# Performance work log

Hardware: AMD Instinct MI355X
Metric: run time of the kernel (lower is better)

Reference implementation:

```python
import jax, jax.numpy as jnp
import numpy as np

BN_EPS = 1e-5
LRELU_SLOPE = 0.2  # CBL = Conv1d(k=1) + BatchNorm1d + LeakyReLU


def three_nn(xyz1, xyz2):
    # xyz1: (B,N,3), xyz2: (B,M,3) -> squared dists (B,N,3), idx (B,N,3)
    d2 = (jnp.sum(xyz1 ** 2, -1, keepdims=True)
          + jnp.sum(xyz2 ** 2, -1)[:, None, :]
          - 2.0 * jnp.einsum('bnd,bmd->bnm', xyz1, xyz2))  # (B,N,M)
    neg, idx = jax.lax.top_k(-d2, 3)
    return -neg, idx


def three_interpolate(points2, idx, weight):
    # points2: (B,C,M), idx: (B,N,3), weight: (B,N,3) -> (B,C,N)
    gathered = jax.vmap(lambda p, i: p[:, i])(points2, idx)  # (B,C,N,3)
    return jnp.einsum('bcnk,bnk->bcn', gathered, weight)


def cbl(x, W, b, gamma, beta):
    # x: (B,C,N); 1x1 conv -> BN (training-mode stats) -> LeakyReLU
    y = jnp.einsum('oc,bcn->bon', W, x) + b[None, :, None]
    mean = jnp.mean(y, axis=(0, 2), keepdims=True)
    var = jnp.var(y, axis=(0, 2), keepdims=True)
    y = (y - mean) * jax.lax.rsqrt(var + BN_EPS)
    y = gamma[None, :, None] * y + beta[None, :, None]
    return jnp.where(y >= 0, y, LRELU_SLOPE * y)


def setup_inputs() -> dict:
    key = jax.random.key(0)
    ks = jax.random.split(key, 8)
    B, N, M = 4, 8192, 2048
    C1, C2 = 128, 256
    Cin = C2 + C1  # use_points1=True -> concat
    H = 256
    return {
        'xyz1': jax.random.normal(ks[0], (B, N, 3), jnp.float32),
        'xyz2': jax.random.normal(ks[1], (B, M, 3), jnp.float32),
        'points1': jax.random.normal(ks[2], (B, C1, N), jnp.float32),
        'points2': jax.random.normal(ks[3], (B, C2, M), jnp.float32),
        'W1': jax.random.normal(ks[4], (H, Cin), jnp.float32) * (1.0 / np.sqrt(Cin)),
        'b1': jnp.zeros((H,), jnp.float32),
        'gamma1': jnp.ones((H,), jnp.float32),
        'beta1': jnp.zeros((H,), jnp.float32),
        'W2': jax.random.normal(ks[5], (H, H), jnp.float32) * (1.0 / np.sqrt(H)),
        'b2': jnp.zeros((H,), jnp.float32),
        'gamma2': jnp.ones((H,), jnp.float32),
        'beta2': jnp.zeros((H,), jnp.float32),
    }


def reference(xyz1, xyz2, points1, points2, W1, b1, gamma1, beta1, W2, b2, gamma2, beta2):
    dist, idx = three_nn(xyz1, xyz2)
    dist = jnp.maximum(dist, 1e-10)
    recip = 1.0 / dist
    weight = recip / jnp.sum(recip, axis=2, keepdims=True)  # (B,N,3)
    interp = three_interpolate(points2, idx, weight)        # (B,C2,N)
    new_points = jnp.concatenate([interp, points1], axis=1)  # (B,C2+C1,N)
    new_points = cbl(new_points, W1, b1, gamma1, beta1)
    new_points = cbl(new_points, W2, b2, gamma2, beta2)
    return new_points
```

## Files before the change

### kernel.cpp

```cpp
#include <hip/hip_runtime.h>
#include <math.h>

constexpr int B   = 4;
constexpr int N   = 8192;
constexpr int M   = 2048;
constexpr int C1  = 128;
constexpr int C2  = 256;
constexpr int HCH = 256;
constexpr int CIN = 384;
constexpr float BN_EPS = 1e-5f;
constexpr float SLOPE  = 0.2f;
constexpr float BN_CNT = (float)(B * N);

__global__ void k_zero(float* __restrict__ stats) {
  int i = blockIdx.x * blockDim.x + threadIdx.x;
  if (i < 1024) stats[i] = 0.f;
}

__global__ __launch_bounds__(256) void k_nn(const float* __restrict__ xyz1,
                                            const float* __restrict__ xyz2,
                                            float* __restrict__ wgt,
                                            int* __restrict__ idxo) {
  __shared__ float4 q[4][512];
  __shared__ float  md[4][64][3];
  __shared__ int    mi[4][64][3];
  const int tid = threadIdx.x;
  const int b   = blockIdx.y;
  const int n0  = blockIdx.x * 64;

  const float* src = xyz2 + (size_t)b * M * 3;
  for (int i = tid; i < M; i += 256) {
    float x = src[i*3+0], y = src[i*3+1], z = src[i*3+2];
    q[i >> 9][i & 511] = make_float4(x, y, z, x*x + y*y + z*z);
  }
  __syncthreads();

  const int w = tid >> 6;
  const int t = tid & 63;
  const int n = n0 + t;
  const float* p = xyz1 + ((size_t)b * N + n) * 3;
  const float px = p[0], py = p[1], pz = p[2];
  const float n1 = px*px + py*py + pz*pz;

  float d0 = 3.4e38f, d1 = 3.4e38f, d2 = 3.4e38f;
  int   j0 = 0, j1 = 0, j2 = 0;
  const float4* qs = q[w];
  #pragma unroll 4
  for (int r = 0; r < 512; ++r) {
    float4 c = qs[r];
    float dot = px*c.x + py*c.y + pz*c.z;
    float d = fmaf(-2.f, dot, n1 + c.w);
    if (d < d2) {
      int m = (w << 9) + r;
      if (d < d1) {
        if (d < d0) { d2 = d1; j2 = j1; d1 = d0; j1 = j0; d0 = d; j0 = m; }
        else        { d2 = d1; j2 = j1; d1 = d;  j1 = m; }
      } else        { d2 = d;  j2 = m; }
    }
  }
  md[w][t][0] = d0; md[w][t][1] = d1; md[w][t][2] = d2;
  mi[w][t][0] = j0; mi[w][t][1] = j1; mi[w][t][2] = j2;
  __syncthreads();

  if (tid < 64) {
    float e0 = 3.4e38f, e1 = 3.4e38f, e2 = 3.4e38f;
    int   i0 = 0, i1 = 0, i2 = 0;
    #pragma unroll
    for (int s = 0; s < 4; ++s) {
      #pragma unroll
      for (int k = 0; k < 3; ++k) {
        float d = md[s][tid][k];
        int   m = mi[s][tid][k];
        if (d < e2) {
          if (d < e1) {
            if (d < e0) { e2 = e1; i2 = i1; e1 = e0; i1 = i0; e0 = d; i0 = m; }
            else        { e2 = e1; i2 = i1; e1 = d;  i1 = m; }
          } else        { e2 = d;  i2 = m; }
        }
      }
    }
    e0 = fmaxf(e0, 1e-10f); e1 = fmaxf(e1, 1e-10f); e2 = fmaxf(e2, 1e-10f);
    float r0 = 1.f / e0, r1 = 1.f / e1, r2 = 1.f / e2;
    float s  = r0 + r1 + r2;
    size_t base = ((size_t)b * N + n0 + tid) * 3;
    wgt[base+0] = r0 / s;  wgt[base+1] = r1 / s;  wgt[base+2] = r2 / s;
    idxo[base+0] = i0;     idxo[base+1] = i1;     idxo[base+2] = i2;
  }
}

__global__ __launch_bounds__(256) void k_tr(const float* __restrict__ P2,
                                            float* __restrict__ P2T) {
  __shared__ float t[32][33];
  const int b  = blockIdx.z;
  const int m0 = blockIdx.x * 32;
  const int c0 = blockIdx.y * 32;
  const int tx = threadIdx.x & 31;
  const int ty = threadIdx.x >> 5;
  const float* src = P2 + (size_t)b * C2 * M;
  #pragma unroll
  for (int j = 0; j < 4; ++j)
    t[ty + j*8][tx] = src[(size_t)(c0 + ty + j*8) * M + m0 + tx];
  __syncthreads();
  float* dst = P2T + (size_t)b * M * C2;
  #pragma unroll
  for (int j = 0; j < 4; ++j)
    dst[(size_t)(m0 + ty + j*8) * C2 + c0 + tx] = t[tx][ty + j*8];
}

__global__ __launch_bounds__(256) void k_interp(const float* __restrict__ P2T,
                                                const float* __restrict__ points1,
                                                const float* __restrict__ wgt,
                                                const int* __restrict__ idx,
                                                float* __restrict__ X) {
  const int b = blockIdx.y;
  const int n = blockIdx.x * 256 + threadIdx.x;
  const size_t base = (size_t)b * N + n;
  const int i0 = idx[base*3+0], i1 = idx[base*3+1], i2 = idx[base*3+2];
  const float w0 = wgt[base*3+0], w1 = wgt[base*3+1], w2 = wgt[base*3+2];
  const float4* r0 = (const float4*)(P2T + ((size_t)b * M + i0) * C2);
  const float4* r1 = (const float4*)(P2T + ((size_t)b * M + i1) * C2);
  const float4* r2 = (const float4*)(P2T + ((size_t)b * M + i2) * C2);
  float* Xb = X + (size_t)b * CIN * N + n;
  #pragma unroll 4
  for (int c4 = 0; c4 < C2/4; ++c4) {
    float4 a0 = r0[c4], a1 = r1[c4], a2 = r2[c4];
    Xb[(size_t)(c4*4+0) * N] = w0*a0.x + w1*a1.x + w2*a2.x;
    Xb[(size_t)(c4*4+1) * N] = w0*a0.y + w1*a1.y + w2*a2.y;
    Xb[(size_t)(c4*4+2) * N] = w0*a0.z + w1*a1.z + w2*a2.z;
    Xb[(size_t)(c4*4+3) * N] = w0*a0.w + w1*a1.w + w2*a2.w;
  }
  const float* p1 = points1 + (size_t)b * C1 * N + n;
  float* Xc = Xb + (size_t)C2 * N;
  #pragma unroll 4
  for (int c = 0; c < C1; ++c) Xc[(size_t)c * N] = p1[(size_t)c * N];
}

template <int K, bool XFORM>
__global__ __launch_bounds__(256) void k_gemm(const float* __restrict__ Wm,
                                              const float* __restrict__ bias,
                                              const float* __restrict__ Xin,
                                              const float* __restrict__ coef,
                                              float* __restrict__ Yout,
                                              float* __restrict__ stats) {
  constexpr int BK = 32;
  __shared__ float Wt[BK][64];
  __shared__ float Xt[BK][64];
  const int tid = threadIdx.x;
  const int tx = tid & 15, ty = tid >> 4;
  const int n0 = blockIdx.x * 64;
  const int o0 = blockIdx.y * 64;
  const int b  = blockIdx.z;
  const float* Xb = Xin + (size_t)b * K * N;

  float acc[4][4] = {};

  for (int k0 = 0; k0 < K; k0 += BK) {
    {
      const int o  = tid >> 2;
      const int kk = (tid & 3) * 8;
      const float* wp = Wm + (size_t)(o0 + o) * K + k0 + kk;
      float4 wv0 = *(const float4*)(wp);
      float4 wv1 = *(const float4*)(wp + 4);
      Wt[kk+0][o] = wv0.x; Wt[kk+1][o] = wv0.y; Wt[kk+2][o] = wv0.z; Wt[kk+3][o] = wv0.w;
      Wt[kk+4][o] = wv1.x; Wt[kk+5][o] = wv1.y; Wt[kk+6][o] = wv1.z; Wt[kk+7][o] = wv1.w;
    }
    {
      const int k  = tid >> 3;
      const int nn = (tid & 7) * 8;
      const float* xp = Xb + (size_t)(k0 + k) * N + n0 + nn;
      float4 x0 = *(const float4*)(xp);
      float4 x1 = *(const float4*)(xp + 4);
      if constexpr (XFORM) {
        const float a  = coef[k0 + k];
        const float bb = coef[256 + k0 + k];
        float t;
        t = fmaf(a, x0.x, bb); x0.x = t >= 0.f ? t : SLOPE * t;
        t = fmaf(a, x0.y, bb); x0.y = t >= 0.f ? t : SLOPE * t;
        t = fmaf(a, x0.z, bb); x0.z = t >= 0.f ? t : SLOPE * t;
        t = fmaf(a, x0.w, bb); x0.w = t >= 0.f ? t : SLOPE * t;
        t = fmaf(a, x1.x, bb); x1.x = t >= 0.f ? t : SLOPE * t;
        t = fmaf(a, x1.y, bb); x1.y = t >= 0.f ? t : SLOPE * t;
        t = fmaf(a, x1.z, bb); x1.z = t >= 0.f ? t : SLOPE * t;
        t = fmaf(a, x1.w, bb); x1.w = t >= 0.f ? t : SLOPE * t;
      }
      *(float4*)&Xt[k][nn]     = x0;
      *(float4*)&Xt[k][nn + 4] = x1;
    }
    __syncthreads();
    #pragma unroll
    for (int kk = 0; kk < BK; ++kk) {
      float4 av = *(const float4*)&Wt[kk][ty * 4];
      float4 bv = *(const float4*)&Xt[kk][tx * 4];
      acc[0][0] = fmaf(av.x, bv.x, acc[0][0]);
      acc[0][1] = fmaf(av.x, bv.y, acc[0][1]);
      acc[0][2] = fmaf(av.x, bv.z, acc[0][2]);
      acc[0][3] = fmaf(av.x, bv.w, acc[0][3]);
      acc[1][0] = fmaf(av.y, bv.x, acc[1][0]);
      acc[1][1] = fmaf(av.y, bv.y, acc[1][1]);
      acc[1][2] = fmaf(av.y, bv.z, acc[1][2]);
      acc[1][3] = fmaf(av.y, bv.w, acc[1][3]);
      acc[2][0] = fmaf(av.z, bv.x, acc[2][0]);
      acc[2][1] = fmaf(av.z, bv.y, acc[2][1]);
      acc[2][2] = fmaf(av.z, bv.z, acc[2][2]);
      acc[2][3] = fmaf(av.z, bv.w, acc[2][3]);
      acc[3][0] = fmaf(av.w, bv.x, acc[3][0]);
      acc[3][1] = fmaf(av.w, bv.y, acc[3][1]);
      acc[3][2] = fmaf(av.w, bv.z, acc[3][2]);
      acc[3][3] = fmaf(av.w, bv.w, acc[3][3]);
    }
    __syncthreads();
  }

  #pragma unroll
  for (int i = 0; i < 4; ++i) {
    const int o = o0 + ty * 4 + i;
    const float bi = bias[o];
    float4 v = make_float4(acc[i][0] + bi, acc[i][1] + bi, acc[i][2] + bi, acc[i][3] + bi);
    *(float4*)&Yout[((size_t)b * HCH + o) * N + n0 + tx * 4] = v;
    float s = v.x + v.y + v.z + v.w;
    float qq = v.x*v.x + v.y*v.y + v.z*v.z + v.w*v.w;
    #pragma unroll
    for (int off = 1; off < 16; off <<= 1) {
      s  += __shfl_xor(s, off);
      qq += __shfl_xor(qq, off);
    }
    if (tx == 0) {
      atomicAdd(&stats[o], s);
      atomicAdd(&stats[256 + o], qq);
    }
  }
}

__global__ void k_fin(const float* __restrict__ stats,
                      const float* __restrict__ gamma,
                      const float* __restrict__ beta,
                      float* __restrict__ coef) {
  const int c = threadIdx.x;
  const float mean = stats[c] / BN_CNT;
  const float var  = stats[256 + c] / BN_CNT - mean * mean;
  const float a    = gamma[c] / sqrtf(var + BN_EPS);
  coef[c]       = a;
  coef[256 + c] = fmaf(-a, mean, beta[c]);
}

__global__ __launch_bounds__(256) void k_apply(const float* __restrict__ Y,
                                               const float* __restrict__ coef,
                                               float* __restrict__ out) {
  const size_t total = (size_t)B * HCH * N / 4;
  const float4* y4 = (const float4*)Y;
  float4* o4 = (float4*)out;
  for (size_t f = (size_t)blockIdx.x * blockDim.x + threadIdx.x; f < total;
       f += (size_t)gridDim.x * blockDim.x) {
    const int c = (int)((f / (N / 4)) % HCH);
    const float a = coef[c], bb = coef[256 + c];
    float4 v = y4[f];
    float t;
    t = fmaf(a, v.x, bb); v.x = t >= 0.f ? t : SLOPE * t;
    t = fmaf(a, v.y, bb); v.y = t >= 0.f ? t : SLOPE * t;
    t = fmaf(a, v.z, bb); v.z = t >= 0.f ? t : SLOPE * t;
    t = fmaf(a, v.w, bb); v.w = t >= 0.f ? t : SLOPE * t;
    o4[f] = v;
  }
}

extern "C" void kernel_launch(void* const* d_in, const int* in_sizes, int n_in,
                              void* d_out, int out_size, void* d_ws, size_t ws_size,
                              hipStream_t stream) {
  const float* xyz1    = (const float*)d_in[0];
  const float* xyz2    = (const float*)d_in[1];
  const float* points1 = (const float*)d_in[2];
  const float* points2 = (const float*)d_in[3];
  const float* W1      = (const float*)d_in[4];
  const float* b1      = (const float*)d_in[5];
  const float* gamma1  = (const float*)d_in[6];
  const float* beta1   = (const float*)d_in[7];
  const float* W2      = (const float*)d_in[8];
  const float* b2      = (const float*)d_in[9];
  const float* gamma2  = (const float*)d_in[10];
  const float* beta2   = (const float*)d_in[11];

  float* ws = (float*)d_ws;
  float* wgt    = ws;
  int*   idx    = (int*)(ws + (size_t)B * N * 3);
  float* P2T    = ws + 2 * (size_t)B * N * 3;
  float* Xbuf   = P2T + (size_t)B * M * C2;
  float* Y1     = Xbuf + (size_t)B * CIN * N;
  float* Y2     = Xbuf;
  float* stats1 = Y1 + (size_t)B * HCH * N;
  float* stats2 = stats1 + 512;
  float* coef1  = stats2 + 512;
  float* coef2  = coef1 + 512;

  k_zero<<<4, 256, 0, stream>>>(stats1);
  k_nn<<<dim3(N / 64, B), 256, 0, stream>>>(xyz1, xyz2, wgt, idx);
  k_tr<<<dim3(M / 32, C2 / 32, B), 256, 0, stream>>>(points2, P2T);
  k_interp<<<dim3(N / 256, B), 256, 0, stream>>>(P2T, points1, wgt, idx, Xbuf);
  k_gemm<CIN, false><<<dim3(N / 64, HCH / 64, B), 256, 0, stream>>>(W1, b1, Xbuf, nullptr, Y1, stats1);
  k_fin<<<1, 256, 0, stream>>>(stats1, gamma1, beta1, coef1);
  k_gemm<HCH, true><<<dim3(N / 64, HCH / 64, B), 256, 0, stream>>>(W2, b2, Y1, coef1, Y2, stats2);
  k_fin<<<1, 256, 0, stream>>>(stats2, gamma2, beta2, coef2);
  k_apply<<<2048, 256, 0, stream>>>(Y2, coef2, (float*)d_out);
}
```

Baseline: 379.9 us.

## Use split-bf16 MFMA (3-pass) for the 1x1 conv GEMMs with 128x128 tiles

Replaces the scalar FP32 FMA GEMM with MFMA bf16 instructions, splitting each fp32 operand into high and low bf16 parts and accumulating three products to approximate fp32 accuracy. Tiles grow to 128x128 with four waves each computing a 64x64 sub-tile, and shared memory is padded to reduce bank conflicts. The X tile is now loaded column-strided per thread (16 scalar loads across k rows), which may reduce coalescing, and the conversion adds ALU work. The accuracy loss from dropping the low-low term is small but nonzero.

Measured after the change: 399.5 us. 5.2% more time.

```diff
diff --git a/kernel.cpp b/kernel.cpp
--- a/kernel.cpp
+++ b/kernel.cpp
@@ -11,6 +11,20 @@
 constexpr float BN_EPS = 1e-5f;
 constexpr float SLOPE  = 0.2f;
 constexpr float BN_CNT = (float)(B * N);
+
+typedef __attribute__((ext_vector_type(8))) short short8;
+typedef __attribute__((ext_vector_type(4))) float f32x4;
+
+__device__ __forceinline__ unsigned short bfh(float x) {
+  unsigned int u = __float_as_uint(x);
+  return (unsigned short)((u + 0x7fffu + ((u >> 16) & 1u)) >> 16);
+}
+__device__ __forceinline__ float bf2f(unsigned short h) {
+  return __uint_as_float((unsigned int)h << 16);
+}
+__device__ __forceinline__ unsigned int pk(unsigned short a, unsigned short b) {
+  return (unsigned int)a | ((unsigned int)b << 16);
+}
 
 __global__ void k_zero(float* __restrict__ stats) {
   int i = blockIdx.x * blockDim.x + threadIdx.x;
@@ -136,97 +150,123 @@
 }
 
 template <int K, bool XFORM>
-__global__ __launch_bounds__(256) void k_gemm(const float* __restrict__ Wm,
-                                              const float* __restrict__ bias,
-                                              const float* __restrict__ Xin,
-                                              const float* __restrict__ coef,
-                                              float* __restrict__ Yout,
-                                              float* __restrict__ stats) {
-  constexpr int BK = 32;
-  __shared__ float Wt[BK][64];
-  __shared__ float Xt[BK][64];
+__global__ __launch_bounds__(256, 2) void k_gemm(const float* __restrict__ Wm,
+                                                 const float* __restrict__ bias,
+                                                 const float* __restrict__ Xin,
+                                                 const float* __restrict__ coef,
+                                                 float* __restrict__ Yout,
+                                                 float* __restrict__ stats) {
+  constexpr int BM = 128, BN = 128, BK = 32, RL = 40;
+  __shared__ unsigned short Wh[BM*RL], Wl[BM*RL], Xh[BN*RL], Xl[BN*RL];
+
   const int tid = threadIdx.x;
-  const int tx = tid & 15, ty = tid >> 4;
-  const int n0 = blockIdx.x * 64;
-  const int o0 = blockIdx.y * 64;
+  const int n0 = blockIdx.x * BN;
+  const int o0 = blockIdx.y * BM;
   const int b  = blockIdx.z;
   const float* Xb = Xin + (size_t)b * K * N;
 
-  float acc[4][4] = {};
+  const int sr = tid >> 1;
+  const int kh = (tid & 1) * 16;
+
+  const int lane = tid & 63;
+  const int wv = tid >> 6;
+  const int wm = wv >> 1, wn = wv & 1;
+  const int lr = lane & 15;
+  const int lk = (lane >> 4) * 8;
+
+  f32x4 acc[4][4] = {};
 
   for (int k0 = 0; k0 < K; k0 += BK) {
     {
-      const int o  = tid >> 2;
-      const int kk = (tid & 3) * 8;
-      const float* wp = Wm + (size_t)(o0 + o) * K + k0 + kk;
-      float4 wv0 = *(const float4*)(wp);
-      float4 wv1 = *(const float4*)(wp + 4);
-      Wt[kk+0][o] = wv0.x; Wt[kk+1][o] = wv0.y; Wt[kk+2][o] = wv0.z; Wt[kk+3][o] = wv0.w;
-      Wt[kk+4][o] = wv1.x; Wt[kk+5][o] = wv1.y; Wt[kk+6][o] = wv1.z; Wt[kk+7][o] = wv1.w;
+      const float* wp = Wm + (size_t)(o0 + sr) * K + k0 + kh;
+      float xv[16];
+      *(float4*)&xv[0]  = *(const float4*)(wp + 0);
+      *(float4*)&xv[4]  = *(const float4*)(wp + 4);
+      *(float4*)&xv[8]  = *(const float4*)(wp + 8);
+      *(float4*)&xv[12] = *(const float4*)(wp + 12);
+      unsigned short h[16], l[16];
+      #pragma unroll
+      for (int i = 0; i < 16; ++i) {
+        h[i] = bfh(xv[i]);
+        l[i] = bfh(xv[i] - bf2f(h[i]));
+      }
+      uint4* dh = (uint4*)&Wh[sr*RL + kh];
+      uint4* dl = (uint4*)&Wl[sr*RL + kh];
+      dh[0] = make_uint4(pk(h[0],h[1]),  pk(h[2],h[3]),  pk(h[4],h[5]),  pk(h[6],h[7]));
+      dh[1] = make_uint4(pk(h[8],h[9]),  pk(h[10],h[11]),pk(h[12],h[13]),pk(h[14],h[15]));
+      dl[0] = make_uint4(pk(l[0],l[1]),  pk(l[2],l[3]),  pk(l[4],l[5]),  pk(l[6],l[7]));
+      dl[1] = make_uint4(pk(l[8],l[9]),  pk(l[10],l[11]),pk(l[12],l[13]),pk(l[14],l[15]));
     }
     {
-      const int k  = tid >> 3;
-      const int nn = (tid & 7) * 8;
-      const float* xp = Xb + (size_t)(k0 + k) * N + n0 + nn;
-      float4 x0 = *(const float4*)(xp);
-      float4 x1 = *(const float4*)(xp + 4);
+      float xv[16];
+      #pragma unroll
+      for (int i = 0; i < 16; ++i)
+        xv[i] = Xb[(size_t)(k0 + kh + i) * N + n0 + sr];
       if constexpr (XFORM) {
-        const float a  = coef[k0 + k];
-        const float bb = coef[256 + k0 + k];
-        float t;
-        t = fmaf(a, x0.x, bb); x0.x = t >= 0.f ? t : SLOPE * t;
-        t = fmaf(a, x0.y, bb); x0.y = t >= 0.f ? t : SLOPE * t;
-        t = fmaf(a, x0.z, bb); x0.z = t >= 0.f ? t : SLOPE * t;
-        t = fmaf(a, x0.w, bb); x0.w = t >= 0.f ? t : SLOPE * t;
-        t = fmaf(a, x1.x, bb); x1.x = t >= 0.f ? t : SLOPE * t;
-        t = fmaf(a, x1.y, bb); x1.y = t >= 0.f ? t : SLOPE * t;
-        t = fmaf(a, x1.z, bb); x1.z = t >= 0.f ? t : SLOPE * t;
-        t = fmaf(a, x1.w, bb); x1.w = t >= 0.f ? t : SLOPE * t;
-      }
-      *(float4*)&Xt[k][nn]     = x0;
-      *(float4*)&Xt[k][nn + 4] = x1;
+        #pragma unroll
+        for (int i = 0; i < 16; ++i) {
+          const int c = k0 + kh + i;
+          float t = fmaf(coef[c], xv[i], coef[256 + c]);
+          xv[i] = t >= 0.f ? t : SLOPE * t;
+        }
+      }
+      unsigned short h[16], l[16];
+      #pragma unroll
+      for (int i = 0; i < 16; ++i) {
+        h[i] = bfh(xv[i]);
+        l[i] = bfh(xv[i] - bf2f(h[i]));
+      }
+      uint4* dh = (uint4*)&Xh[sr*RL + kh];
+      uint4* dl = (uint4*)&Xl[sr*RL + kh];
+      dh[0] = make_uint4(pk(h[0],h[1]),  pk(h[2],h[3]),  pk(h[4],h[5]),  pk(h[6],h[7]));
+      dh[1] = make_uint4(pk(h[8],h[9]),  pk(h[10],h[11]),pk(h[12],h[13]),pk(h[14],h[15]));
+      dl[0] = make_uint4(pk(l[0],l[1]),  pk(l[2],l[3]),  pk(l[4],l[5]),  pk(l[6],l[7]));
+      dl[1] = make_uint4(pk(l[8],l[9]),  pk(l[10],l[11]),pk(l[12],l[13]),pk(l[14],l[15]));
     }
     __syncthreads();
+
+    short8 bh[4], bl[4];
     #pragma unroll
-    for (int kk = 0; kk < BK; ++kk) {
-      float4 av = *(const float4*)&Wt[kk][ty * 4];
-      float4 bv = *(const float4*)&Xt[kk][tx * 4];
-      acc[0][0] = fmaf(av.x, bv.x, acc[0][0]);
-      acc[0][1] = fmaf(av.x, bv.y, acc[0][1]);
-      acc[0][2] = fmaf(av.x, bv.z, acc[0][2]);
-      acc[0][3] = fmaf(av.x, bv.w, acc[0][3]);
-      acc[1][0] = fmaf(av.y, bv.x, acc[1][0]);
-      acc[1][1] = fmaf(av.y, bv.y, acc[1][1]);
-      acc[1][2] = fmaf(av.y, bv.z, acc[1][2]);
-      acc[1][3] = fmaf(av.y, bv.w, acc[1][3]);
-      acc[2][0] = fmaf(av.z, bv.x, acc[2][0]);
-      acc[2][1] = fmaf(av.z, bv.y, acc[2][1]);
-      acc[2][2] = fmaf(av.z, bv.z, acc[2][2]);
-      acc[2][3] = fmaf(av.z, bv.w, acc[2][3]);
-      acc[3][0] = fmaf(av.w, bv.x, acc[3][0]);
-      acc[3][1] = fmaf(av.w, bv.y, acc[3][1]);
-      acc[3][2] = fmaf(av.w, bv.z, acc[3][2]);
-      acc[3][3] = fmaf(av.w, bv.w, acc[3][3]);
+    for (int n = 0; n < 4; ++n) {
+      bh[n] = *(const short8*)&Xh[(wn*64 + n*16 + lr)*RL + lk];
+      bl[n] = *(const short8*)&Xl[(wn*64 + n*16 + lr)*RL + lk];
+    }
+    #pragma unroll
+    for (int m = 0; m < 4; ++m) {
+      short8 ah = *(const short8*)&Wh[(wm*64 + m*16 + lr)*RL + lk];
+      short8 al = *(const short8*)&Wl[(wm*64 + m*16 + lr)*RL + lk];
+      #pragma unroll
+      for (int n = 0; n < 4; ++n) {
+        acc[m][n] = __builtin_amdgcn_mfma_f32_16x16x32_bf16(ah, bh[n], acc[m][n], 0, 0, 0);
+        acc[m][n] = __builtin_amdgcn_mfma_f32_16x16x32_bf16(ah, bl[n], acc[m][n], 0, 0, 0);
+        acc[m][n] = __builtin_amdgcn_mfma_f32_16x16x32_bf16(al, bh[n], acc[m][n], 0, 0, 0);
+      }
     }
     __syncthreads();
   }
 
   #pragma unroll
-  for (int i = 0; i < 4; ++i) {
-    const int o = o0 + ty * 4 + i;
-    const float bi = bias[o];
-    float4 v = make_float4(acc[i][0] + bi, acc[i][1] + bi, acc[i][2] + bi, acc[i][3] + bi);
-    *(float4*)&Yout[((size_t)b * HCH + o) * N + n0 + tx * 4] = v;
-    float s = v.x + v.y + v.z + v.w;
-    float qq = v.x*v.x + v.y*v.y + v.z*v.z + v.w*v.w;
+  for (int m = 0; m < 4; ++m) {
     #pragma unroll
-    for (int off = 1; off < 16; off <<= 1) {
-      s  += __shfl_xor(s, off);
-      qq += __shfl_xor(qq, off);
-    }
-    if (tx == 0) {
-      atomicAdd(&stats[o], s);
-      atomicAdd(&stats[256 + o], qq);
+    for (int r = 0; r < 4; ++r) {
+      const int o = o0 + wm*64 + m*16 + (lane >> 4)*4 + r;
+      const float bi = bias[o];
+      float s = 0.f, q = 0.f;
+      #pragma unroll
+      for (int n = 0; n < 4; ++n) {
+        float v = acc[m][n][r] + bi;
+        Yout[((size_t)b * HCH + o) * N + n0 + wn*64 + n*16 + lr] = v;
+        s += v; q += v*v;
+      }
+      #pragma unroll
+      for (int off = 1; off < 16; off <<= 1) {
+        s += __shfl_xor(s, off);
+        q += __shfl_xor(q, off);
+      }
+      if (lr == 0) {
+        atomicAdd(&stats[o], s);
+        atomicAdd(&stats[256 + o], q);
+      }
     }
   }
 }
@@ -295,9 +335,9 @@
   k_nn<<<dim3(N / 64, B), 256, 0, stream>>>(xyz1, xyz2, wgt, idx);
   k_tr<<<dim3(M / 32, C2 / 32, B), 256, 0, stream>>>(points2, P2T);
   k_interp<<<dim3(N / 256, B), 256, 0, stream>>>(P2T, points1, wgt, idx, Xbuf);
-  k_gemm<CIN, false><<<dim3(N / 64, HCH / 64, B), 256, 0, stream>>>(W1, b1, Xbuf, nullptr, Y1, stats1);
+  k_gemm<CIN, false><<<dim3(N / 128, HCH / 128, B), 256, 0, stream>>>(W1, b1, Xbuf, nullptr, Y1, stats1);
   k_fin<<<1, 256, 0, stream>>>(stats1, gamma1, beta1, coef1);
-  k_gemm<HCH, true><<<dim3(N / 64, HCH / 64, B), 256, 0, stream>>>(W2, b2, Y1, coef1, Y2, stats2);
+  k_gemm<HCH, true><<<dim3(N / 128, HCH / 128, B), 256, 0, stream>>>(W2, b2, Y1, coef1, Y2, stats2);
   k_fin<<<1, 256, 0, stream>>>(stats2, gamma2, beta2, coef2);
   k_apply<<<2048, 256, 0, stream>>>(Y2, coef2, (float*)d_out);
 }
```
